# Kernel tuning notes

Measured on AMD Instinct MI355X. Metric: run time of the kernel, lower is better.

Reference implementation:

```python
import jax, jax.numpy as jnp
import numpy as np

NENTITY = 200000
NRELATION = 500
HIDDEN = 256
GAMMA = 12.0
EPS = 2.0
EMB_RANGE = (GAMMA + EPS) / HIDDEN


def setup_inputs() -> dict:
    key = jax.random.key(0)
    ks = jax.random.split(key, 8)
    B, NEG = 256, 1024
    head = jax.random.randint(ks[0], (B, 1), 0, NENTITY)
    tail = jax.random.randint(ks[1], (B, NEG), 0, NENTITY)
    relation = jax.random.randint(ks[2], (B,), 0, NRELATION)
    entity_emb = jax.random.uniform(ks[3], (NENTITY, HIDDEN), jnp.float32, -EMB_RANGE, EMB_RANGE)
    relation_emb = jax.random.uniform(ks[4], (NRELATION, 2 * HIDDEN), jnp.float32, -EMB_RANGE, EMB_RANGE)
    lim = 1.0 / np.sqrt(2 * HIDDEN)
    W_fc = jax.random.uniform(ks[5], (HIDDEN, 2 * HIDDEN), jnp.float32, -lim, lim)
    b_fc = jax.random.uniform(ks[6], (HIDDEN,), jnp.float32, -lim, lim)
    return {"head": head, "tail": tail, "relation": relation,
            "entity_emb": entity_emb, "relation_emb": relation_emb,
            "W_fc": W_fc, "b_fc": b_fc}


def _l2_normalize(x):
    # F.normalize(x, p=2, dim=-1): x / max(||x||_2, 1e-12)
    n = jnp.sqrt(jnp.sum(x * x, axis=-1, keepdims=True))
    return x / jnp.maximum(n, 1e-12)


def reference(head, tail, relation, entity_emb, relation_emb, W_fc, b_fc):
    # gather embeddings
    h = entity_emb[head]                      # [B, 1,   d]
    t = entity_emb[tail]                      # [B, NEG, d]
    r = relation_emb[relation][:, None, :]    # [B, 1, 2d]
    re_head, re_tail = jnp.split(r, 2, axis=-1)   # each [B, 1, d]
    # broadcast relation halves to match head/tail sample counts, then concat
    re_h = jnp.broadcast_to(re_head, h.shape)
    re_t = jnp.broadcast_to(re_tail, t.shape)
    h_cat = jnp.concatenate([h, re_h], axis=-1)   # [B, 1,   2d]
    t_cat = jnp.concatenate([t, re_t], axis=-1)   # [B, NEG, 2d]
    # shared small FC (torch Linear: x @ W^T + b)
    h_fc = jnp.einsum('bnk,dk->bnd', h_cat, W_fc) + b_fc
    t_fc = jnp.einsum('bnk,dk->bnd', t_cat, W_fc) + b_fc
    h_n = _l2_normalize(h_fc)
    t_n = _l2_normalize(t_fc)
    diff = h_n - t_n                              # [B, NEG, d]
    score = GAMMA - jnp.sum(jnp.abs(diff), axis=2)  # [B, NEG]
    return score
```

## Files before the change

kernel.cpp:

```cpp
#include <hip/hip_runtime.h>
#include <math.h>

#define HIDDEN 256
#define NEG 1024
#define NBATCH 256
#define GAMMA_F 12.0f
#define BM 32
#define NTILES 8
#define NBLK 1024

typedef short v8s __attribute__((ext_vector_type(8)));
typedef float v4f __attribute__((ext_vector_type(4)));
typedef unsigned int u32;

#define LDS_BARRIER() asm volatile("s_waitcnt lgkmcnt(0)\n\ts_barrier" ::: "memory")

__device__ __forceinline__ short f2bf(float x) {
    u32 u = __float_as_uint(x);
    u = (u + 0x7fffu + ((u >> 16) & 1u)) >> 16;
    return (short)u;
}

__device__ __forceinline__ u32 rhu(float f) { return __float_as_uint(f) + 0x8000u; }
__device__ __forceinline__ v8s pack8(const float4& x0, const float4& x1) {
    int4 fr;
    fr.x = __builtin_amdgcn_perm(rhu(x0.y), rhu(x0.x), 0x07060302u);
    fr.y = __builtin_amdgcn_perm(rhu(x0.w), rhu(x0.z), 0x07060302u);
    fr.z = __builtin_amdgcn_perm(rhu(x1.y), rhu(x1.x), 0x07060302u);
    fr.w = __builtin_amdgcn_perm(rhu(x1.w), rhu(x1.z), 0x07060302u);
    return __builtin_bit_cast(v8s, fr);
}

__global__ __launch_bounds__(256) void prep_kernel(
    const int* __restrict__ head, const int* __restrict__ relation,
    const float* __restrict__ entity_emb, const float* __restrict__ relation_emb,
    const float* __restrict__ W_fc, const float* __restrict__ b_fc,
    short* __restrict__ W1bf, float* __restrict__ h_n, float* __restrict__ rel_part)
{
    const int b = blockIdx.x;
    const int t = threadIdx.x;

    W1bf[b * HIDDEN + t] = f2bf(W_fc[(size_t)b * 2 * HIDDEN + t]);

    __shared__ float xh[2 * HIDDEN];
    __shared__ float xt[HIDDEN];
    __shared__ float red[256];

    const int hidx = head[b];
    const int r = relation[b];
    xh[t]          = entity_emb[(size_t)hidx * HIDDEN + t];
    xh[HIDDEN + t] = relation_emb[(size_t)r * 2 * HIDDEN + t];
    xt[t]          = relation_emb[(size_t)r * 2 * HIDDEN + HIDDEN + t];
    __syncthreads();

    const float4* wrow = reinterpret_cast<const float4*>(W_fc + (size_t)t * 2 * HIDDEN);
    float hf = b_fc[t];
    float rp = b_fc[t];
    #pragma unroll 4
    for (int kk = 0; kk < HIDDEN / 4; ++kk) {
        float4 w = wrow[kk];
        hf += xh[4*kk+0]*w.x + xh[4*kk+1]*w.y + xh[4*kk+2]*w.z + xh[4*kk+3]*w.w;
    }
    #pragma unroll 4
    for (int kk = 0; kk < HIDDEN / 4; ++kk) {
        float4 w = wrow[HIDDEN/4 + kk];
        hf += xh[HIDDEN+4*kk+0]*w.x + xh[HIDDEN+4*kk+1]*w.y + xh[HIDDEN+4*kk+2]*w.z + xh[HIDDEN+4*kk+3]*w.w;
        rp += xt[4*kk+0]*w.x + xt[4*kk+1]*w.y + xt[4*kk+2]*w.z + xt[4*kk+3]*w.w;
    }
    rel_part[b * HIDDEN + t] = rp;

    red[t] = hf * hf;
    __syncthreads();
    for (int s = 128; s > 0; s >>= 1) {
        if (t < s) red[t] += red[t + s];
        __syncthreads();
    }
    const float norm = sqrtf(red[0]);
    h_n[b * HIDDEN + t] = hf / fmaxf(norm, 1e-12f);
}

__global__ __launch_bounds__(256, 2) void score_kernel(
    const int* __restrict__ tail, const float* __restrict__ entity_emb,
    const short* __restrict__ W1bf, const float* __restrict__ h_n,
    const float* __restrict__ rel_part, float* __restrict__ out)
{
    __shared__ __align__(16) float Asf[2][BM * HIDDEN];
    __shared__ int tails[NTILES * BM];
    __shared__ float ssq_lds[4][BM];
    __shared__ float l1_lds[4][BM];

    const int t = threadIdx.x;
    const int w = t >> 6;
    const int l = t & 63;
    const int c = t & 15;
    const int g = (t >> 4) & 3;
    const int b = blockIdx.x >> 2;

    tails[t] = tail[blockIdx.x * (NTILES * BM) + t];

    float rlv[4], hnv[4];
    #pragma unroll
    for (int ntl = 0; ntl < 4; ++ntl) {
        const int n = 64 * w + ntl * 16 + c;
        rlv[ntl] = rel_part[b * HIDDEN + n];
        hnv[ntl] = h_n[b * HIDDEN + n];
    }

    v8s Bf[4][8];
    #pragma unroll
    for (int ntl = 0; ntl < 4; ++ntl) {
        const short* bsrc = W1bf + (size_t)(64 * w + ntl * 16 + c) * HIDDEN + g * 8;
        #pragma unroll
        for (int kt = 0; kt < 8; ++kt)
            Bf[ntl][kt] = *reinterpret_cast<const v8s*>(bsrc + kt * 32);
    }

    __syncthreads();

    auto issue = [&](int j, int buf) {
        #pragma unroll
        for (int i = 0; i < 8; ++i) {
            const int r = w * 8 + i;
            const int row = tails[j * BM + r];
            const float* src = entity_emb + (size_t)row * HIDDEN + ((l ^ (r & 7)) << 2);
            __builtin_amdgcn_global_load_lds(
                (const __attribute__((address_space(1))) u32*)src,
                (__attribute__((address_space(3))) u32*)&Asf[buf][r * HIDDEN],
                16, 0, 0);
        }
    };

    issue(0, 0);

    #pragma unroll 1
    for (int j = 0; j < NTILES; ++j) {
        const int cur = j & 1;

        if (j + 1 < NTILES) {
            issue(j + 1, cur ^ 1);
            asm volatile("s_waitcnt vmcnt(8)" ::: "memory");
        } else {
            asm volatile("s_waitcnt vmcnt(0)" ::: "memory");
        }
        asm volatile("s_barrier" ::: "memory");

        v4f acc[2][4];
        #pragma unroll
        for (int mt = 0; mt < 2; ++mt)
            #pragma unroll
            for (int ntl = 0; ntl < 4; ++ntl)
                acc[mt][ntl] = v4f{0.f, 0.f, 0.f, 0.f};

        const float* a0base = &Asf[cur][c * HIDDEN];
        const float* a1base = &Asf[cur][(16 + c) * HIDDEN];
        const int swz = c & 7;

        #pragma unroll
        for (int kt = 0; kt < 8; ++kt) {
            const int u0 = kt * 8 + g * 2;
            float4 x0 = *reinterpret_cast<const float4*>(a0base + (((u0    ) ^ swz) << 2));
            float4 x1 = *reinterpret_cast<const float4*>(a0base + (((u0 + 1) ^ swz) << 2));
            float4 y0 = *reinterpret_cast<const float4*>(a1base + (((u0    ) ^ swz) << 2));
            float4 y1 = *reinterpret_cast<const float4*>(a1base + (((u0 + 1) ^ swz) << 2));
            v8s a0 = pack8(x0, x1);
            v8s a1 = pack8(y0, y1);
            #pragma unroll
            for (int ntl = 0; ntl < 4; ++ntl) {
                acc[0][ntl] = __builtin_amdgcn_mfma_f32_16x16x32_bf16(a0, Bf[ntl][kt], acc[0][ntl], 0, 0, 0);
                acc[1][ntl] = __builtin_amdgcn_mfma_f32_16x16x32_bf16(a1, Bf[ntl][kt], acc[1][ntl], 0, 0, 0);
            }
        }

        #pragma unroll
        for (int mt = 0; mt < 2; ++mt) {
            float ssq[4] = {0.f, 0.f, 0.f, 0.f};
            #pragma unroll
            for (int ntl = 0; ntl < 4; ++ntl) {
                #pragma unroll
                for (int r = 0; r < 4; ++r) {
                    float tf = acc[mt][ntl][r] + rlv[ntl];
                    acc[mt][ntl][r] = tf;
                    ssq[r] += tf * tf;
                }
            }
            #pragma unroll
            for (int mask = 1; mask < 16; mask <<= 1) {
                #pragma unroll
                for (int r = 0; r < 4; ++r) ssq[r] += __shfl_xor(ssq[r], mask);
            }
            if (c == 0) {
                #pragma unroll
                for (int r = 0; r < 4; ++r) ssq_lds[w][mt * 16 + g * 4 + r] = ssq[r];
            }
        }
        LDS_BARRIER();

        #pragma unroll
        for (int mt = 0; mt < 2; ++mt) {
            float rn[4], s1[4] = {0.f, 0.f, 0.f, 0.f};
            #pragma unroll
            for (int r = 0; r < 4; ++r) {
                const int m = mt * 16 + g * 4 + r;
                float tot = ssq_lds[0][m] + ssq_lds[1][m] + ssq_lds[2][m] + ssq_lds[3][m];
                rn[r] = 1.f / fmaxf(sqrtf(tot), 1e-12f);
            }
            #pragma unroll
            for (int ntl = 0; ntl < 4; ++ntl) {
                #pragma unroll
                for (int r = 0; r < 4; ++r)
                    s1[r] += fabsf(hnv[ntl] - acc[mt][ntl][r] * rn[r]);
            }
            #pragma unroll
            for (int mask = 1; mask < 16; mask <<= 1) {
                #pragma unroll
                for (int r = 0; r < 4; ++r) s1[r] += __shfl_xor(s1[r], mask);
            }
            if (c == 0) {
                #pragma unroll
                for (int r = 0; r < 4; ++r) l1_lds[w][mt * 16 + g * 4 + r] = s1[r];
            }
        }
        LDS_BARRIER();

        if (t < BM) {
            out[blockIdx.x * (NTILES * BM) + j * BM + t] = GAMMA_F -
                (l1_lds[0][t] + l1_lds[1][t] + l1_lds[2][t] + l1_lds[3][t]);
        }
    }
}

extern "C" void kernel_launch(void* const* d_in, const int* in_sizes, int n_in,
                              void* d_out, int out_size, void* d_ws, size_t ws_size,
                              hipStream_t stream)
{
    const int*   head         = (const int*)d_in[0];
    const int*   tail         = (const int*)d_in[1];
    const int*   relation     = (const int*)d_in[2];
    const float* entity_emb   = (const float*)d_in[3];
    const float* relation_emb = (const float*)d_in[4];
    const float* W_fc         = (const float*)d_in[5];
    const float* b_fc         = (const float*)d_in[6];
    float* out = (float*)d_out;

    short* W1bf     = (short*)d_ws;
    float* h_n      = (float*)((char*)d_ws + 131072);
    float* rel_part = (float*)((char*)d_ws + 131072 + 262144);

    prep_kernel<<<NBATCH, 256, 0, stream>>>(head, relation, entity_emb, relation_emb,
                                            W_fc, b_fc, W1bf, h_n, rel_part);
    score_kernel<<<NBLK, 256, 0, stream>>>(tail, entity_emb, W1bf,
                                           h_n, rel_part, out);
}
```

Measured before the change: 349.7 us.

## Prefetch tail rows into registers instead of direct global-to-LDS loads

Replaces the asynchronous global_load_lds double-buffer with register-staged prefetch. The next tile's rows are loaded into VGPRs before compute and written to the alternate LDS buffer after compute, with the XOR swizzle applied on the LDS store. This drops the per-iteration vmcnt wait and barrier before compute, and the data is not needed until after the MFMA work. It costs 8 extra v4f registers per thread, which may reduce occupancy, and adds a separate LDS write pass.

```diff
diff --git a/kernel.cpp b/kernel.cpp
--- a/kernel.cpp
+++ b/kernel.cpp
@@ -117,32 +117,33 @@
 
     __syncthreads();
 
-    auto issue = [&](int j, int buf) {
+    v4f st[8];
+    auto issue = [&](int j) {
         #pragma unroll
         for (int i = 0; i < 8; ++i) {
             const int r = w * 8 + i;
-            const int row = tails[j * BM + r];
-            const float* src = entity_emb + (size_t)row * HIDDEN + ((l ^ (r & 7)) << 2);
-            __builtin_amdgcn_global_load_lds(
-                (const __attribute__((address_space(1))) u32*)src,
-                (__attribute__((address_space(3))) u32*)&Asf[buf][r * HIDDEN],
-                16, 0, 0);
-        }
+            const float* src = entity_emb + (size_t)tails[j * BM + r] * HIDDEN + (l << 2);
+            st[i] = *reinterpret_cast<const v4f*>(src);
+        }
+        __builtin_amdgcn_sched_barrier(0);
     };
-
-    issue(0, 0);
+    auto commit = [&](int buf) {
+        #pragma unroll
+        for (int i = 0; i < 8; ++i) {
+            const int r = w * 8 + i;
+            *reinterpret_cast<v4f*>(&Asf[buf][r * HIDDEN + ((l ^ (r & 7)) << 2)]) = st[i];
+        }
+    };
+
+    issue(0);
+    commit(0);
+    LDS_BARRIER();
 
     #pragma unroll 1
     for (int j = 0; j < NTILES; ++j) {
         const int cur = j & 1;
 
-        if (j + 1 < NTILES) {
-            issue(j + 1, cur ^ 1);
-            asm volatile("s_waitcnt vmcnt(8)" ::: "memory");
-        } else {
-            asm volatile("s_waitcnt vmcnt(0)" ::: "memory");
-        }
-        asm volatile("s_barrier" ::: "memory");
+        if (j + 1 < NTILES) issue(j + 1);
 
         v4f acc[2][4];
         #pragma unroll
@@ -220,6 +221,8 @@
                 for (int r = 0; r < 4; ++r) l1_lds[w][mt * 16 + g * 4 + r] = s1[r];
             }
         }
+
+        if (j + 1 < NTILES) commit(cur ^ 1);
         LDS_BARRIER();
 
         if (t < BM) {
```

Measured after the change: 362.9 us. 1.04x slower.
